# Performance work log

Hardware: AMD Instinct MI355X
Metric: run time of the kernel (lower is better)

## Reference

```python
import jax, jax.numpy as jnp
import numpy as np

CLS_ID = 0
CONF_THRES = 0.25
IOU_THRES = 0.45
MAX_DET = 300
TOPK = 300  # candidates entering greedy NMS (score-sorted)


def setup_inputs() -> dict:
    key = jax.random.key(0)
    x = jax.random.uniform(key, (16, 25200, 85), dtype=jnp.float32)
    # make xywh realistic for a 640x640 image so IoU suppression is meaningful
    xy = x[..., 0:2] * 640.0
    wh = x[..., 2:4] * 64.0 + 4.0
    rest = x[..., 4:]  # objectness + 80 class probs in [0,1]
    return {"YOLOoutput": jnp.concatenate([xy, wh, rest], axis=-1)}


def _xywh2xyxy(b):
    xy, wh = b[..., 0:2], b[..., 2:4]
    return jnp.concatenate([xy - wh * 0.5, xy + wh * 0.5], axis=-1)


def _iou_one_vs_all(box, boxes):
    # box: [4], boxes: [K,4] (xyxy)
    lt = jnp.maximum(box[:2], boxes[:, :2])
    rb = jnp.minimum(box[2:], boxes[:, 2:])
    wh = jnp.clip(rb - lt, 0.0)
    inter = wh[:, 0] * wh[:, 1]
    a1 = (box[2] - box[0]) * (box[3] - box[1])
    a2 = (boxes[:, 2] - boxes[:, 0]) * (boxes[:, 3] - boxes[:, 1])
    return inter / (a1 + a2 - inter + 1e-9)


def _per_image(pred):
    # pred: [N, 5+C]
    obj = pred[:, 4]
    scores = obj[:, None] * pred[:, 5:]            # [N, C] conf = obj * cls
    conf = scores.max(axis=-1)
    j = scores.argmax(axis=-1)
    valid = (obj > CONF_THRES) & (conf > CONF_THRES) & (j == CLS_ID)
    s = jnp.where(valid, conf, -1.0)
    top_s, idx = jax.lax.top_k(s, TOPK)            # sorted descending
    boxes = _xywh2xyxy(pred[idx, :4])              # [TOPK, 4]
    vmask = top_s > 0.0

    def body(keep, i):
        ious = _iou_one_vs_all(boxes[i], boxes)    # [TOPK]
        supp = (ious > IOU_THRES) & (jnp.arange(TOPK) > i) & keep[i]
        return keep & ~supp, None

    keep, _ = jax.lax.scan(body, vmask, jnp.arange(TOPK))
    rank = jnp.cumsum(keep) - 1
    keep = keep & (rank < MAX_DET)
    cnt = keep.sum().astype(jnp.float32)
    mean_conf = jnp.where(keep, top_s, 0.0).sum() / jnp.maximum(cnt, 1.0)
    return jnp.where(cnt > 0, mean_conf, 0.0)


def reference(YOLOoutput):
    # per-image mean detection confidence for class CLS_ID; 0.0 where no dets
    return jax.vmap(_per_image)(YOLOoutput)
```

## Files before the change

### kernel.cpp

```cpp
#include <hip/hip_runtime.h>

#define NIMG   16
#define NA     25200
#define NCH    85
#define NCLS   80
#define CAP    2048
#define TOPK_N 300
#define CONF_T 0.25f
#define IOU_T  0.45f

#define CHUNK  128
#define FBLK   256
#define NBLK   512
#define NWORDS 5

__global__ __launch_bounds__(FBLK) void filter_kernel(
    const float* __restrict__ pred, int* __restrict__ cnt,
    unsigned long long* __restrict__ keys)
{
    __shared__ float lds[CHUNK * NCH];

    const int blocks_per_img = (NA + CHUNK - 1) / CHUNK;
    int img   = blockIdx.x / blocks_per_img;
    int chunk = blockIdx.x % blocks_per_img;
    int a0    = chunk * CHUNK;
    int count = min(CHUNK, NA - a0);

    const float4* src = reinterpret_cast<const float4*>(pred + ((size_t)img * NA + a0) * NCH);
    float4* dst = reinterpret_cast<float4*>(lds);
    int nf4 = count * NCH / 4;
    for (int i = threadIdx.x; i < nf4; i += FBLK) dst[i] = src[i];
    __syncthreads();

    int t = threadIdx.x;
    if (t < count) {
        const float* p = &lds[t * NCH];
        float obj = p[4];
        if (obj > CONF_T) {
            float best = -1.0f; int bestj = -1;
            #pragma unroll 8
            for (int j = 0; j < NCLS; ++j) {
                float s = obj * p[5 + j];
                if (s > best) { best = s; bestj = j; }
            }
            if (bestj == 0 && best > CONF_T) {
                int pos = atomicAdd(&cnt[img], 1);
                if (pos < CAP) {
                    unsigned cb = __float_as_uint(best);
                    unsigned a  = (unsigned)(a0 + t);
                    keys[(size_t)img * CAP + pos] =
                        ((unsigned long long)cb << 32) | (unsigned long long)(0xFFFFFFFFu - a);
                }
            }
        }
    }
}

__global__ __launch_bounds__(NBLK) void nms_kernel(
    const float* __restrict__ pred, const int* __restrict__ cnt,
    const unsigned long long* __restrict__ keys_g, float* __restrict__ out)
{
    __shared__ unsigned long long keys[CAP];
    __shared__ float bx1[TOPK_N], by1[TOPK_N], bx2[TOPK_N], by2[TOPK_N], bconf[TOPK_N];
    __shared__ unsigned long long mask[TOPK_N * NWORDS];
    __shared__ unsigned long long keepw[NWORDS];
    __shared__ float rsum[NBLK / 64];
    __shared__ int   rcnt[NBLK / 64];

    int img = blockIdx.x;
    int tid = threadIdx.x;
    int n = min(cnt[img], CAP);

    int N = 1; while (N < n) N <<= 1;
    for (int i = tid; i < N; i += NBLK)
        keys[i] = (i < n) ? keys_g[(size_t)img * CAP + i] : 0ULL;
    __syncthreads();
    for (int k = 2; k <= N; k <<= 1) {
        for (int j = k >> 1; j > 0; j >>= 1) {
            for (int i = tid; i < N; i += NBLK) {
                int p = i ^ j;
                if (p > i) {
                    unsigned long long a = keys[i], b = keys[p];
                    bool desc = ((i & k) == 0);
                    if ((a < b) == desc) { keys[i] = b; keys[p] = a; }
                }
            }
            __syncthreads();
        }
    }

    int m = min(n, TOPK_N);

    if (tid < m) {
        unsigned long long kk = keys[tid];
        unsigned a = 0xFFFFFFFFu - (unsigned)(kk & 0xFFFFFFFFu);
        float conf = __uint_as_float((unsigned)(kk >> 32));
        const float* p = pred + ((size_t)img * NA + a) * NCH;
        float x = p[0], y = p[1], w = p[2], h = p[3];
        bx1[tid] = x - w * 0.5f;
        by1[tid] = y - h * 0.5f;
        bx2[tid] = x + w * 0.5f;
        by2[tid] = y + h * 0.5f;
        bconf[tid] = conf;
    }
    __syncthreads();

    for (int idx = tid; idx < m * NWORDS; idx += NBLK) {
        int i = idx / NWORDS, w = idx % NWORDS;
        unsigned long long bits = 0ULL;
        int jlo = w * 64, jhi = min(jlo + 64, m);
        if (jhi > i + 1) {
            float ax1 = bx1[i], ay1 = by1[i], ax2 = bx2[i], ay2 = by2[i];
            float a1 = (ax2 - ax1) * (ay2 - ay1);
            for (int j = max(jlo, i + 1); j < jhi; ++j) {
                float ltx = fmaxf(ax1, bx1[j]);
                float lty = fmaxf(ay1, by1[j]);
                float rbx = fminf(ax2, bx2[j]);
                float rby = fminf(ay2, by2[j]);
                float ww = fmaxf(rbx - ltx, 0.0f);
                float hh = fmaxf(rby - lty, 0.0f);
                float inter = ww * hh;
                float a2 = (bx2[j] - bx1[j]) * (by2[j] - by1[j]);
                float iou = inter / (a1 + a2 - inter + 1e-9f);
                if (iou > IOU_T) bits |= 1ULL << (j - jlo);
            }
        }
        mask[i * NWORDS + w] = bits;
    }
    __syncthreads();

    if (tid < 64) {
        int lane = tid;
        unsigned long long kw = 0ULL;
        if (lane < NWORDS) {
            int rem = m - lane * 64;
            kw = (rem >= 64) ? ~0ULL : ((rem <= 0) ? 0ULL : ((1ULL << rem) - 1ULL));
        }
        for (int i = 0; i < m; ++i) {
            unsigned long long wi = __shfl(kw, i >> 6);
            if ((wi >> (i & 63)) & 1ULL) {
                unsigned long long mw = (lane < NWORDS) ? mask[i * NWORDS + lane] : 0ULL;
                kw &= ~mw;
            }
        }
        if (lane < NWORDS) keepw[lane] = kw;
    }
    __syncthreads();

    float s = 0.0f; int c = 0;
    if (tid < m) {
        if ((keepw[tid >> 6] >> (tid & 63)) & 1ULL) { s = bconf[tid]; c = 1; }
    }
    for (int off = 32; off > 0; off >>= 1) {
        s += __shfl_down(s, off);
        c += __shfl_down(c, off);
    }
    int wid = tid >> 6;
    if ((tid & 63) == 0) { rsum[wid] = s; rcnt[wid] = c; }
    __syncthreads();
    if (tid == 0) {
        float S = 0.0f; int C = 0;
        for (int wv = 0; wv < NBLK / 64; ++wv) { S += rsum[wv]; C += rcnt[wv]; }
        out[img] = (C > 0) ? S / (float)C : 0.0f;
    }
}

extern "C" void kernel_launch(void* const* d_in, const int* in_sizes, int n_in,
                              void* d_out, int out_size, void* d_ws, size_t ws_size,
                              hipStream_t stream) {
    const float* pred = (const float*)d_in[0];
    float* out = (float*)d_out;

    int* cnt = (int*)d_ws;
    unsigned long long* keys = (unsigned long long*)((char*)d_ws + 256);

    hipMemsetAsync(d_ws, 0, 256, stream);

    const int blocks_per_img = (NA + CHUNK - 1) / CHUNK;
    filter_kernel<<<NIMG * blocks_per_img, FBLK, 0, stream>>>(pred, cnt, keys);
    nms_kernel<<<NIMG, NBLK, 0, stream>>>(pred, cnt, keys, out);
}
```

Measured before the change: 122.1 us.

## Read anchors directly and early-exit filter on objectness and class-0 score

The filter kernel no longer stages a whole chunk of the prediction tensor in LDS. Each thread now reads its own anchor straight from global memory and exits as soon as objectness or the class-0 score fails the threshold, or as soon as any group of 8 classes beats class 0. The aim is to avoid loading all 85 channels for the many anchors that get rejected early, cutting HBM traffic. The trade-off is strided, uncoalesced per-thread loads in place of coalesced float4 staging. Ties between class 0 and another class are now resolved as in argmax (first index wins), so the result stays equivalent.

```diff
diff --git a/kernel.cpp b/kernel.cpp
--- a/kernel.cpp
+++ b/kernel.cpp
@@ -9,7 +9,6 @@
 #define CONF_T 0.25f
 #define IOU_T  0.45f
 
-#define CHUNK  128
 #define FBLK   256
 #define NBLK   512
 #define NWORDS 5
@@ -18,41 +17,34 @@
     const float* __restrict__ pred, int* __restrict__ cnt,
     unsigned long long* __restrict__ keys)
 {
-    __shared__ float lds[CHUNK * NCH];
+    int a = blockIdx.x * FBLK + threadIdx.x;
+    if (a >= NA) return;
+    int img = blockIdx.y;
+    const float* __restrict__ p = pred + ((size_t)img * NA + a) * NCH;
 
-    const int blocks_per_img = (NA + CHUNK - 1) / CHUNK;
-    int img   = blockIdx.x / blocks_per_img;
-    int chunk = blockIdx.x % blocks_per_img;
-    int a0    = chunk * CHUNK;
-    int count = min(CHUNK, NA - a0);
+    float obj = p[4];
+    if (obj <= CONF_T) return;
+    float s0 = obj * p[5];
+    if (s0 <= CONF_T) return;
 
-    const float4* src = reinterpret_cast<const float4*>(pred + ((size_t)img * NA + a0) * NCH);
-    float4* dst = reinterpret_cast<float4*>(lds);
-    int nf4 = count * NCH / 4;
-    for (int i = threadIdx.x; i < nf4; i += FBLK) dst[i] = src[i];
-    __syncthreads();
-
-    int t = threadIdx.x;
-    if (t < count) {
-        const float* p = &lds[t * NCH];
-        float obj = p[4];
-        if (obj > CONF_T) {
-            float best = -1.0f; int bestj = -1;
-            #pragma unroll 8
-            for (int j = 0; j < NCLS; ++j) {
+    for (int j0 = 1; j0 < NCLS; j0 += 8) {
+        int jn = min(j0 + 8, NCLS);
+        float mx = -1.0f;
+        #pragma unroll
+        for (int j = j0; j < j0 + 8; ++j) {
+            if (j < jn) {
                 float s = obj * p[5 + j];
-                if (s > best) { best = s; bestj = j; }
-            }
-            if (bestj == 0 && best > CONF_T) {
-                int pos = atomicAdd(&cnt[img], 1);
-                if (pos < CAP) {
-                    unsigned cb = __float_as_uint(best);
-                    unsigned a  = (unsigned)(a0 + t);
-                    keys[(size_t)img * CAP + pos] =
-                        ((unsigned long long)cb << 32) | (unsigned long long)(0xFFFFFFFFu - a);
-                }
+                mx = fmaxf(mx, s);
             }
         }
+        if (mx > s0) return;
+    }
+
+    int pos = atomicAdd(&cnt[img], 1);
+    if (pos < CAP) {
+        unsigned cb = __float_as_uint(s0);
+        keys[(size_t)img * CAP + pos] =
+            ((unsigned long long)cb << 32) | (unsigned long long)(0xFFFFFFFFu - (unsigned)a);
     }
 }
 
@@ -78,11 +70,11 @@
     for (int k = 2; k <= N; k <<= 1) {
         for (int j = k >> 1; j > 0; j >>= 1) {
             for (int i = tid; i < N; i += NBLK) {
-                int p = i ^ j;
-                if (p > i) {
-                    unsigned long long a = keys[i], b = keys[p];
+                int pp = i ^ j;
+                if (pp > i) {
+                    unsigned long long va = keys[i], vb = keys[pp];
                     bool desc = ((i & k) == 0);
-                    if ((a < b) == desc) { keys[i] = b; keys[p] = a; }
+                    if ((va < vb) == desc) { keys[i] = vb; keys[pp] = va; }
                 }
             }
             __syncthreads();
@@ -176,7 +168,7 @@
 
     hipMemsetAsync(d_ws, 0, 256, stream);
 
-    const int blocks_per_img = (NA + CHUNK - 1) / CHUNK;
-    filter_kernel<<<NIMG * blocks_per_img, FBLK, 0, stream>>>(pred, cnt, keys);
+    dim3 fgrid((NA + FBLK - 1) / FBLK, NIMG);
+    filter_kernel<<<fgrid, FBLK, 0, stream>>>(pred, cnt, keys);
     nms_kernel<<<NIMG, NBLK, 0, stream>>>(pred, cnt, keys, out);
 }
```

New measurement: 122.1 us. No clear change (+0.0%).
